# Performance work log

Measured on AMD Instinct MI355X. Metric: run time of the kernel, lower is better.

Reference implementation:

```python
import jax, jax.numpy as jnp
import numpy as np

B, S, D, H, W = 2, 2048, 1024, 16, 128
HD = D // H


def setup_inputs() -> dict:
    key = jax.random.key(0)
    ks = jax.random.split(key, 9)
    s = 1.0 / np.sqrt(D)
    return {
        "x": jax.random.normal(ks[0], (B, S, D), jnp.float32),
        "Wq": jax.random.normal(ks[1], (D, D), jnp.float32) * s,
        "bq": jax.random.normal(ks[2], (D,), jnp.float32) * 0.01,
        "Wk": jax.random.normal(ks[3], (D, D), jnp.float32) * s,
        "bk": jax.random.normal(ks[4], (D,), jnp.float32) * 0.01,
        "Wv": jax.random.normal(ks[5], (D, D), jnp.float32) * s,
        "bv": jax.random.normal(ks[6], (D,), jnp.float32) * 0.01,
        "Wo": jax.random.normal(ks[7], (D, D), jnp.float32) * s,
        "bo": jax.random.normal(ks[8], (D,), jnp.float32) * 0.01,
    }


def reference(x, Wq, bq, Wk, bk, Wv, bv, Wo, bo):
    b, s, d = x.shape
    # projections (torch Linear: x @ W.T + b)
    q = (jnp.einsum('bsd,ed->bse', x, Wq) + bq).reshape(b, s, H, HD).transpose(0, 2, 1, 3)
    k = (jnp.einsum('bsd,ed->bse', x, Wk) + bk).reshape(b, s, H, HD).transpose(0, 2, 1, 3)
    v = (jnp.einsum('bsd,ed->bse', x, Wv) + bv).reshape(b, s, H, HD).transpose(0, 2, 1, 3)
    scores = jnp.einsum('bhqd,bhkd->bhqk', q, k) / jnp.sqrt(jnp.asarray(HD, x.dtype))
    # local band mask: mask[i, j] = 1 iff i - W//2 <= j <= i + W//2
    idx = jnp.arange(s)
    band = jnp.abs(idx[:, None] - idx[None, :]) <= (W // 2)  # [S, S]
    scores = jnp.where(band[None, None], scores, -jnp.inf)
    attn = jax.nn.softmax(scores, axis=-1)  # dropout is identity in eval
    ctx = jnp.einsum('bhqk,bhkd->bqhd', attn, v).reshape(b, s, d)
    out = jnp.einsum('bsd,ed->bse', ctx, Wo) + bo
    return out, attn
```

## Files before the change

kernel.cpp:

```cpp
#include <hip/hip_runtime.h>
#include <math.h>
#include <stdint.h>

typedef _Float16 f16;
typedef f16   f16x8 __attribute__((ext_vector_type(8)));
typedef f16   f16x4 __attribute__((ext_vector_type(4)));
typedef float f32x4 __attribute__((ext_vector_type(4)));

constexpr int Bc = 2, Sc = 2048, Dc = 1024, Hc = 16, HDc = 64;
constexpr size_t PROJ = (size_t)Bc * Sc * Dc;
constexpr size_t WN   = (size_t)Dc * Dc;

__device__ __forceinline__ void gload_lds16(const void* g, void* l) {
    unsigned int off = (unsigned int)(uintptr_t)l;
    auto lp = (__attribute__((address_space(3))) unsigned int*)(uintptr_t)off;
    auto gp = (const __attribute__((address_space(1))) unsigned int*)(uintptr_t)g;
    __builtin_amdgcn_global_load_lds(gp, lp, 16, 0, 0);
}

__global__ __launch_bounds__(256)
void pack_all(const float* __restrict__ x,
              const float* __restrict__ w0, const float* __restrict__ w1,
              const float* __restrict__ w2, const float* __restrict__ w3,
              f16* __restrict__ xd, f16* __restrict__ wd) {
    const int bid = blockIdx.x;
    const float* src;
    f16* dst;
    int off4;
    if (bid < 4096) {
        src = x; dst = xd; off4 = bid;
    } else {
        const int wi = (bid - 4096) >> 10;
        const int r  = (bid - 4096) & 1023;
        src = (wi == 0) ? w0 : (wi == 1) ? w1 : (wi == 2) ? w2 : w3;
        dst = wd + (size_t)wi * WN;
        off4 = r;
    }
    const int i = off4 * 256 + threadIdx.x;
    float4 f = ((const float4*)src)[i];
    f16x4 h = {(f16)f.x, (f16)f.y, (f16)f.z, (f16)f.w};
    ((f16x4*)dst)[i] = h;
}

template <typename OutT>
__global__ __launch_bounds__(256, 2)
void gemm_mega(const f16* __restrict__ A, const f16* __restrict__ W,
               const float* __restrict__ b0, const float* __restrict__ b1,
               const float* __restrict__ b2,
               OutT* __restrict__ o0, OutT* __restrict__ o1, OutT* __restrict__ o2,
               float* __restrict__ fill, int n_gemm, int n_ct) {
    constexpr int K = 1024, N = 1024;
    const int bid = blockIdx.x;
    const int t = threadIdx.x;

    if (bid >= n_gemm) {
        uint4* z = (uint4*)fill + (size_t)(bid - n_gemm) * 16384;
        const uint4 zero = {0u, 0u, 0u, 0u};
        #pragma unroll 8
        for (int it = 0; it < 64; ++it)
            z[it * 256 + t] = zero;
        return;
    }

    __shared__ f16 sA[128 * 32];
    __shared__ f16 sB[128 * 32];

    const int w = t >> 6, l = t & 63, l15 = l & 15, quad = l >> 4;
    const int col_t = bid % n_ct, row_t = bid / n_ct;
    const int row0 = row_t * 128, col0 = col_t * 128;
    const int wr = w >> 1, wc = w & 1;

    f32x4 acc[4][4];
    #pragma unroll
    for (int i = 0; i < 4; ++i)
        #pragma unroll
        for (int j = 0; j < 4; ++j) acc[i][j] = (f32x4){0.f, 0.f, 0.f, 0.f};

    const int arow = t >> 2;
    const int koff = (t & 3) * 8;
    const f16* ga = A + (size_t)(row0 + arow) * K + koff;
    const f16* gb = W + (size_t)(col0 + arow) * K + koff;
    f16* lA1 = sA + w * 512;
    f16* lA2 = sA + 2048 + w * 512;
    f16* lB1 = sB + w * 512;
    f16* lB2 = sB + 2048 + w * 512;

    for (int k0 = 0; k0 < K; k0 += 32) {
        gload_lds16(ga + k0, lA1);
        gload_lds16(ga + (size_t)64 * K + k0, lA2);
        gload_lds16(gb + k0, lB1);
        gload_lds16(gb + (size_t)64 * K + k0, lB2);
        __syncthreads();

        f16x8 af[4], bf[4];
        #pragma unroll
        for (int mi = 0; mi < 4; ++mi)
            af[mi] = *(const f16x8*)&sA[(wr * 64 + mi * 16 + l15) * 32 + quad * 8];
        #pragma unroll
        for (int ni = 0; ni < 4; ++ni)
            bf[ni] = *(const f16x8*)&sB[(wc * 64 + ni * 16 + l15) * 32 + quad * 8];
        #pragma unroll
        for (int mi = 0; mi < 4; ++mi)
            #pragma unroll
            for (int ni = 0; ni < 4; ++ni)
                acc[mi][ni] = __builtin_amdgcn_mfma_f32_16x16x32_f16(af[mi], bf[ni], acc[mi][ni], 0, 0, 0);
        __syncthreads();
    }

    const int ten = col0 >> 10;
    const float* bias = (ten == 0) ? b0 : (ten == 1) ? b1 : b2;
    OutT* out = (ten == 0) ? o0 : (ten == 1) ? o1 : o2;
    const int nc0 = col0 & (N - 1);

    #pragma unroll
    for (int mi = 0; mi < 4; ++mi)
        #pragma unroll
        for (int ni = 0; ni < 4; ++ni) {
            const int rbase = row0 + wr * 64 + mi * 16 + quad * 4;
            const int col = nc0 + wc * 64 + ni * 16 + l15;
            const float bv = bias[col];
            #pragma unroll
            for (int r = 0; r < 4; ++r)
                out[(size_t)(rbase + r) * N + col] = (OutT)(acc[mi][ni][r] + bv);
        }
}

__global__ __launch_bounds__(256, 2)
void attn_fused(const f16* __restrict__ qb, const f16* __restrict__ kb,
                const f16* __restrict__ vb, float* __restrict__ attn,
                f16* __restrict__ ctx) {
    __shared__ f16 sQ[64 * 72];
    __shared__ f16 sK[192 * 72];
    __shared__ f16 sV[192 * 72];
    f16* sP = sK;

    const int t = threadIdx.x, w = t >> 6, l = t & 63, l15 = l & 15, quad = l >> 4;
    const int bx = blockIdx.x;
    const int tile = bx & 31, h = (bx >> 5) & 15, b = bx >> 9;
    const int q0 = tile * 64;
    const int jbase = q0 - 64;

    const f16* qg = qb + ((size_t)(b * Sc + q0)) * Dc + h * HDc;
    #pragma unroll
    for (int it = 0; it < 2; ++it) {
        const int idx = it * 256 + t;
        const int r = idx >> 3, c = (idx & 7) * 8;
        *(uint4*)&sQ[r * 72 + c] = *(const uint4*)&qg[(size_t)r * Dc + c];
    }
    #pragma unroll
    for (int it = 0; it < 6; ++it) {
        const int idx = it * 256 + t;
        const int r = idx >> 3, c = (idx & 7) * 8;
        int j = jbase + r;
        j = (j < 0) ? 0 : (j > Sc - 1 ? Sc - 1 : j);
        const size_t goff = ((size_t)(b * Sc + j)) * Dc + h * HDc + c;
        *(uint4*)&sK[r * 72 + c] = *(const uint4*)&kb[goff];
        *(uint4*)&sV[r * 72 + c] = *(const uint4*)&vb[goff];
    }
    __syncthreads();

    f32x4 s[12];
    #pragma unroll
    for (int nt = 0; nt < 12; ++nt) s[nt] = (f32x4){0.f, 0.f, 0.f, 0.f};
    #pragma unroll
    for (int kk = 0; kk < 64; kk += 32) {
        const f16x8 aq = *(const f16x8*)&sQ[(w * 16 + l15) * 72 + kk + quad * 8];
        #pragma unroll
        for (int nt = 0; nt < 12; ++nt) {
            const f16x8 bk_ = *(const f16x8*)&sK[(nt * 16 + l15) * 72 + kk + quad * 8];
            s[nt] = __builtin_amdgcn_mfma_f32_16x16x32_f16(aq, bk_, s[nt], 0, 0, 0);
        }
    }

    float invr[4];
    #pragma unroll
    for (int r = 0; r < 4; ++r) {
        const int row = w * 16 + quad * 4 + r;
        const int lo = (row > 64 - q0) ? row : (64 - q0);
        const int hi2 = (row + 128 < 2111 - q0) ? (row + 128) : (2111 - q0);
        float m = -1e30f;
        #pragma unroll
        for (int nt = 0; nt < 12; ++nt) {
            const int jrel = nt * 16 + l15;
            const float v = s[nt][r] * 0.125f;
            if (jrel >= lo && jrel <= hi2) m = fmaxf(m, v);
        }
        #pragma unroll
        for (int k = 1; k < 16; k <<= 1) m = fmaxf(m, __shfl_xor(m, k, 64));
        float sum = 0.f;
        #pragma unroll
        for (int nt = 0; nt < 12; ++nt) {
            const int jrel = nt * 16 + l15;
            const float v = s[nt][r] * 0.125f;
            const float e = (jrel >= lo && jrel <= hi2) ? __expf(v - m) : 0.f;
            s[nt][r] = e;
            sum += e;
        }
        #pragma unroll
        for (int k = 1; k < 16; k <<= 1) sum += __shfl_xor(sum, k, 64);
        invr[r] = 1.f / sum;
    }
    __syncthreads();

    float* abase = attn + ((size_t)(b * Hc + h) * Sc) * Sc;
    #pragma unroll
    for (int r = 0; r < 4; ++r) {
        const int row = w * 16 + quad * 4 + r;
        const int i = q0 + row;
        const int lo = (row > 64 - q0) ? row : (64 - q0);
        const int hi2 = (row + 128 < 2111 - q0) ? (row + 128) : (2111 - q0);
        #pragma unroll
        for (int nt = 0; nt < 12; ++nt) {
            const int jrel = nt * 16 + l15;
            const float p = s[nt][r] * invr[r];
            sP[row * 200 + jrel] = (f16)p;
            if (jrel >= lo && jrel <= hi2)
                abase[(size_t)i * Sc + (jbase + jrel)] = p;
        }
    }
    __syncthreads();

    f32x4 o[4];
    #pragma unroll
    for (int dt = 0; dt < 4; ++dt) o[dt] = (f32x4){0.f, 0.f, 0.f, 0.f};
    #pragma unroll
    for (int ks = 0; ks < 6; ++ks) {
        const f16x8 ap = *(const f16x8*)&sP[(w * 16 + l15) * 200 + ks * 32 + quad * 8];
        #pragma unroll
        for (int dt = 0; dt < 4; ++dt) {
            f16x8 bv;
            #pragma unroll
            for (int jj = 0; jj < 8; ++jj)
                bv[jj] = sV[(ks * 32 + quad * 8 + jj) * 72 + dt * 16 + l15];
            o[dt] = __builtin_amdgcn_mfma_f32_16x16x32_f16(ap, bv, o[dt], 0, 0, 0);
        }
    }
    f16* cg = ctx + ((size_t)(b * Sc + q0)) * Dc + h * HDc;
    #pragma unroll
    for (int dt = 0; dt < 4; ++dt)
        #pragma unroll
        for (int r = 0; r < 4; ++r) {
            const int row = w * 16 + quad * 4 + r;
            cg[(size_t)row * Dc + dt * 16 + l15] = (f16)o[dt][r];
        }
}

extern "C" void kernel_launch(void* const* d_in, const int* in_sizes, int n_in,
                              void* d_out, int out_size, void* d_ws, size_t ws_size,
                              hipStream_t stream) {
    const float* x  = (const float*)d_in[0];
    const float* Wq = (const float*)d_in[1];
    const float* bq = (const float*)d_in[2];
    const float* Wk = (const float*)d_in[3];
    const float* bk = (const float*)d_in[4];
    const float* Wv = (const float*)d_in[5];
    const float* bv = (const float*)d_in[6];
    const float* Wo = (const float*)d_in[7];
    const float* bo = (const float*)d_in[8];

    float* out  = (float*)d_out;
    float* attn = out + PROJ;

    char* ws = (char*)d_ws;
    f16* Wcat  = (f16*)ws;
    f16* x_f16 = (f16*)(ws + (size_t)8  * 1024 * 1024);
    f16* q_f16 = (f16*)(ws + (size_t)16 * 1024 * 1024);
    f16* k_f16 = (f16*)(ws + (size_t)24 * 1024 * 1024);
    f16* v_f16 = (f16*)(ws + (size_t)32 * 1024 * 1024);
    f16* c_f16 = (f16*)(ws + (size_t)40 * 1024 * 1024);

    pack_all<<<dim3(8192), dim3(256), 0, stream>>>(x, Wq, Wk, Wv, Wo, x_f16, Wcat);

    gemm_mega<f16><<<dim3(768 + 2048), dim3(256), 0, stream>>>(
        x_f16, Wcat, bq, bk, bv, q_f16, k_f16, v_f16, attn, 768, 24);

    attn_fused<<<dim3(Bc * Hc * (Sc / 64)), dim3(256), 0, stream>>>(
        q_f16, k_f16, v_f16, attn, c_f16);

    gemm_mega<float><<<dim3(256), dim3(256), 0, stream>>>(
        c_f16, Wcat + 3 * WN, bo, bo, bo, out, out, out, nullptr, 256, 8);
}
```

Measured before the change: 661.3 us.

## Skip zero-filling band region and interleave fill work across GEMM and attention launches

The zero-fill of the attention matrix now writes only the out-of-band columns of each row, rounded to 32-column boundaries. The attention kernel writes the in-band probabilities, including the zeros that pad out to those boundaries, so no element is written twice. The fill rows are split between the QKV GEMM launch and the attention launch, with fill blocks interleaved among compute blocks in groups of eight. This is meant to cut redundant global writes of the large attn output and to overlap memory-bound stores with compute. It adds per-row boundary arithmetic and a more complex block-index mapping.

```diff
diff --git a/kernel.cpp b/kernel.cpp
--- a/kernel.cpp
+++ b/kernel.cpp
@@ -16,6 +16,26 @@
     auto lp = (__attribute__((address_space(3))) unsigned int*)(uintptr_t)off;
     auto gp = (const __attribute__((address_space(1))) unsigned int*)(uintptr_t)g;
     __builtin_amdgcn_global_load_lds(gp, lp, 16, 0, 0);
+}
+
+__device__ __forceinline__ void fill_rows32(float* __restrict__ attn, int grow0, int t) {
+    const uint4 z = {0u, 0u, 0u, 0u};
+    for (int rr = 0; rr < 32; ++rr) {
+        const int gr = grow0 + rr;
+        const int i = gr & (Sc - 1);
+        const int lo = (i > 64) ? (i - 64) : 0;
+        const int a0 = lo & ~31;
+        const int hi = (i < Sc - 65) ? (i + 64) : (Sc - 1);
+        int a1 = (hi + 32) & ~31; if (a1 > Sc) a1 = Sc;
+        uint4* rowp = (uint4*)(attn + (size_t)gr * Sc);
+        const int n4L = a0 >> 2;
+        const int r0  = a1 >> 2;
+        const int tot = n4L + (512 - r0);
+        for (int idx = t; idx < tot; idx += 256) {
+            const int p = (idx < n4L) ? idx : (r0 + idx - n4L);
+            rowp[p] = z;
+        }
+    }
 }
 
 __global__ __launch_bounds__(256)
@@ -42,31 +62,38 @@
     ((f16x4*)dst)[i] = h;
 }
 
-template <typename OutT>
+template <typename OutT, bool WITH_FILL>
 __global__ __launch_bounds__(256, 2)
 void gemm_mega(const f16* __restrict__ A, const f16* __restrict__ W,
                const float* __restrict__ b0, const float* __restrict__ b1,
                const float* __restrict__ b2,
                OutT* __restrict__ o0, OutT* __restrict__ o1, OutT* __restrict__ o2,
-               float* __restrict__ fill, int n_gemm, int n_ct) {
+               float* __restrict__ fill, int n_ct) {
     constexpr int K = 1024, N = 1024;
     const int bid = blockIdx.x;
     const int t = threadIdx.x;
 
-    if (bid >= n_gemm) {
-        uint4* z = (uint4*)fill + (size_t)(bid - n_gemm) * 16384;
-        const uint4 zero = {0u, 0u, 0u, 0u};
-        #pragma unroll 8
-        for (int it = 0; it < 64; ++it)
-            z[it * 256 + t] = zero;
-        return;
+    int gid = bid;
+    if (WITH_FILL) {
+        int fid = -1;
+        if (bid < 1536) {
+            const int g8 = bid >> 3, l8 = bid & 7;
+            if (g8 & 1) fid = (g8 >> 1) * 8 + l8;
+            else        gid = (g8 >> 1) * 8 + l8;
+        } else {
+            fid = 768 + (bid - 1536);
+        }
+        if (fid >= 0) {
+            fill_rows32(fill, fid * 32, t);
+            return;
+        }
     }
 
     __shared__ f16 sA[128 * 32];
     __shared__ f16 sB[128 * 32];
 
     const int w = t >> 6, l = t & 63, l15 = l & 15, quad = l >> 4;
-    const int col_t = bid % n_ct, row_t = bid / n_ct;
+    const int col_t = gid % n_ct, row_t = gid / n_ct;
     const int row0 = row_t * 128, col0 = col_t * 128;
     const int wr = w >> 1, wc = w & 1;
 
@@ -129,14 +156,29 @@
 void attn_fused(const f16* __restrict__ qb, const f16* __restrict__ kb,
                 const f16* __restrict__ vb, float* __restrict__ attn,
                 f16* __restrict__ ctx) {
+    const int bid = blockIdx.x;
+    const int t = threadIdx.x;
+
+    int aid = bid, fid = -1;
+    if (bid < 1536) {
+        const int g8 = bid >> 3, l8 = bid & 7;
+        if (g8 & 1) fid = (g8 >> 1) * 8 + l8;
+        else        aid = (g8 >> 1) * 8 + l8;
+    } else {
+        aid = 768 + (bid - 1536);
+    }
+    if (fid >= 0) {
+        fill_rows32(attn, 40960 + fid * 32, t);
+        return;
+    }
+
     __shared__ f16 sQ[64 * 72];
     __shared__ f16 sK[192 * 72];
     __shared__ f16 sV[192 * 72];
     f16* sP = sK;
 
-    const int t = threadIdx.x, w = t >> 6, l = t & 63, l15 = l & 15, quad = l >> 4;
-    const int bx = blockIdx.x;
-    const int tile = bx & 31, h = (bx >> 5) & 15, b = bx >> 9;
+    const int w = t >> 6, l = t & 63, l15 = l & 15, quad = l >> 4;
+    const int tile = aid & 31, h = (aid >> 5) & 15, b = aid >> 9;
     const int q0 = tile * 64;
     const int jbase = q0 - 64;
 
@@ -207,14 +249,17 @@
     for (int r = 0; r < 4; ++r) {
         const int row = w * 16 + quad * 4 + r;
         const int i = q0 + row;
-        const int lo = (row > 64 - q0) ? row : (64 - q0);
-        const int hi2 = (row + 128 < 2111 - q0) ? (row + 128) : (2111 - q0);
+        const int lo0 = (i > 64) ? (i - 64) : 0;
+        const int a0 = lo0 & ~31;
+        const int hi0 = (i < Sc - 65) ? (i + 64) : (Sc - 1);
+        int a1 = (hi0 + 32) & ~31; if (a1 > Sc) a1 = Sc;
+        const int alo = a0 - jbase, ahi = a1 - jbase;
         #pragma unroll
         for (int nt = 0; nt < 12; ++nt) {
             const int jrel = nt * 16 + l15;
             const float p = s[nt][r] * invr[r];
             sP[row * 200 + jrel] = (f16)p;
-            if (jrel >= lo && jrel <= hi2)
+            if (jrel >= alo && jrel < ahi)
                 abase[(size_t)i * Sc + (jbase + jrel)] = p;
         }
     }
@@ -271,12 +316,12 @@
 
     pack_all<<<dim3(8192), dim3(256), 0, stream>>>(x, Wq, Wk, Wv, Wo, x_f16, Wcat);
 
-    gemm_mega<f16><<<dim3(768 + 2048), dim3(256), 0, stream>>>(
-        x_f16, Wcat, bq, bk, bv, q_f16, k_f16, v_f16, attn, 768, 24);
-
-    attn_fused<<<dim3(Bc * Hc * (Sc / 64)), dim3(256), 0, stream>>>(
+    gemm_mega<f16, true><<<dim3(2048), dim3(256), 0, stream>>>(
+        x_f16, Wcat, bq, bk, bv, q_f16, k_f16, v_f16, attn, 24);
+
+    attn_fused<<<dim3(1792), dim3(256), 0, stream>>>(
         q_f16, k_f16, v_f16, attn, c_f16);
 
-    gemm_mega<float><<<dim3(256), dim3(256), 0, stream>>>(
-        c_f16, Wcat + 3 * WN, bo, bo, bo, out, out, out, nullptr, 256, 8);
-}
+    gemm_mega<float, false><<<dim3(256), dim3(256), 0, stream>>>(
+        c_f16, Wcat + 3 * WN, bo, bo, bo, out, out, out, nullptr, 8);
+}
```

Measured after the change: 645.7 us. -2.4%, faster.
